# Kernel tuning notes

Measured on AMD Instinct MI355X. Metric: run time of the kernel, lower is better.

## Reference

```python
import jax, jax.numpy as jnp
import numpy as np

N, E, G = 50000, 800000, 64
IN_C, HID, HEADS, OUT_C = 128, 64, 4, 10
NEG_SLOPE = 0.2
EPS = 1e-16


def gat_conv(x, src, dst, W, a_src, a_dst, bias, heads, out_ch):
    # x: [N, F_in]; W: [F_in, heads*out_ch]; a_*: [heads, out_ch]; bias: [heads*out_ch]
    n = x.shape[0]
    h = (x @ W).reshape(n, heads, out_ch)                     # [N, H, C]
    alpha_src = jnp.einsum('nhc,hc->nh', h, a_src)            # [N, H]
    alpha_dst = jnp.einsum('nhc,hc->nh', h, a_dst)            # [N, H]
    e = jax.nn.leaky_relu(alpha_src[src] + alpha_dst[dst], NEG_SLOPE)  # [E, H]
    # segment softmax over incoming edges of each destination node
    m = jax.ops.segment_max(e, dst, num_segments=n)
    ex = jnp.exp(e - m[dst])
    denom = jax.ops.segment_sum(ex, dst, num_segments=n)
    alpha = ex / (denom[dst] + EPS)                           # [E, H]
    msg = h[src] * alpha[:, :, None]                          # [E, H, C]
    out = jax.ops.segment_sum(msg, dst, num_segments=n)       # [N, H, C]
    return out.reshape(n, heads * out_ch) + bias


def setup_inputs() -> dict:
    key = jax.random.key(0)
    ks = jax.random.split(key, 16)
    s = 0.1
    inp = {
        'x': jax.random.normal(ks[0], (N, IN_C), dtype=jnp.float32),
        'edge_index': jax.random.randint(ks[1], (2, E), 0, N, dtype=jnp.int64)
            if jax.config.jax_enable_x64 else jax.random.randint(ks[1], (2, E), 0, N).astype(jnp.int32),
        'batch': jnp.sort(jax.random.randint(ks[2], (N,), 0, G).astype(jnp.int32)),
        'W1': s * jax.random.normal(ks[3], (IN_C, HEADS * HID), dtype=jnp.float32),
        'as1': s * jax.random.normal(ks[4], (HEADS, HID), dtype=jnp.float32),
        'ad1': s * jax.random.normal(ks[5], (HEADS, HID), dtype=jnp.float32),
        'b1': jnp.zeros((HEADS * HID,), jnp.float32),
        'W2': s * jax.random.normal(ks[6], (HEADS * HID, HEADS * HID), dtype=jnp.float32),
        'as2': s * jax.random.normal(ks[7], (HEADS, HID), dtype=jnp.float32),
        'ad2': s * jax.random.normal(ks[8], (HEADS, HID), dtype=jnp.float32),
        'b2': jnp.zeros((HEADS * HID,), jnp.float32),
        'W3': s * jax.random.normal(ks[9], (HEADS * HID, HID), dtype=jnp.float32),
        'as3': s * jax.random.normal(ks[10], (1, HID), dtype=jnp.float32),
        'ad3': s * jax.random.normal(ks[11], (1, HID), dtype=jnp.float32),
        'b3': jnp.zeros((HID,), jnp.float32),
        'Wc': s * jax.random.normal(ks[12], (HID, OUT_C), dtype=jnp.float32),
        'bc': jnp.zeros((OUT_C,), jnp.float32),
    }
    return inp


def reference(x, edge_index, batch, W1, as1, ad1, b1, W2, as2, ad2, b2,
              W3, as3, ad3, b3, Wc, bc):
    n = x.shape[0]
    loop = jnp.arange(n, dtype=edge_index.dtype)
    src = jnp.concatenate([edge_index[0], loop])  # add self-loops (PyG default)
    dst = jnp.concatenate([edge_index[1], loop])

    h = gat_conv(x, src, dst, W1, as1, ad1, b1, HEADS, HID)
    h = jax.nn.elu(h)
    h = gat_conv(h, src, dst, W2, as2, ad2, b2, HEADS, HID)
    h = jax.nn.elu(h)
    h = gat_conv(h, src, dst, W3, as3, ad3, b3, 1, HID)

    # global mean pool over graphs
    sums = jax.ops.segment_sum(h, batch, num_segments=G)            # [G, HID]
    counts = jax.ops.segment_sum(jnp.ones((n,), h.dtype), batch, num_segments=G)
    pooled = sums / jnp.maximum(counts, 1.0)[:, None]

    logits = pooled @ Wc + bc                                       # [G, OUT_C]
    return logits
```

## Files before the change

kernel.cpp:

```cpp
#include <hip/hip_runtime.h>

#define NEG_SLOPE 0.2f
#define EPSV 1e-16f
#define BCAP 6144

typedef unsigned short ushort_t;
typedef unsigned char uchar_t;
typedef __attribute__((ext_vector_type(8))) short bf16x8;
typedef __attribute__((ext_vector_type(4))) float f32x4;
typedef __attribute__((ext_vector_type(2))) float f32x2;

__device__ __forceinline__ ushort_t f2bf(float f) {
    union { float f; unsigned u; } v; v.f = f;
    unsigned r = v.u + 0x7FFFu + ((v.u >> 16) & 1u);
    return (ushort_t)(r >> 16);
}
__device__ __forceinline__ float bf2f(ushort_t u) {
    union { unsigned u; float f; } v; v.u = ((unsigned)u) << 16;
    return v.f;
}
__device__ __forceinline__ uchar_t f2fp8(float f) {
    int p = __builtin_amdgcn_cvt_pk_fp8_f32(f, 0.f, 0, false);
    return (uchar_t)(p & 0xff);
}

__global__ __launch_bounds__(256)
void bucketA_kernel(const int* __restrict__ ei, int* __restrict__ gcursor,
                    unsigned* __restrict__ bbuf, int E, int n, int nbuk) {
    __shared__ int hist[256];
    __shared__ int base[256];
    const int t = threadIdx.x;
    const long cb = (long)blockIdx.x * 4096;
    const int M = E + n;
    hist[t] = 0;
    __syncthreads();
    unsigned entry[16];
    int bk[16], lr[16];
    #pragma unroll
    for (int j = 0; j < 16; ++j) {
        long i = cb + j * 256 + t;
        bk[j] = -1;
        if (i < M) {
            int s, d;
            if (i < E) { s = ei[i]; d = ei[E + i]; }
            else       { s = (int)(i - E); d = s; }
            int b = d >> 8;
            bk[j] = b;
            entry[j] = (unsigned)s | ((unsigned)(d & 255) << 16);
            lr[j] = atomicAdd(&hist[b], 1);
        }
    }
    __syncthreads();
    if (t < nbuk && hist[t] > 0) base[t] = atomicAdd(&gcursor[t], hist[t]);
    __syncthreads();
    #pragma unroll
    for (int j = 0; j < 16; ++j)
        if (bk[j] >= 0)
            bbuf[(long)bk[j] * BCAP + base[bk[j]] + lr[j]] = entry[j];
}

__global__ __launch_bounds__(256)
void bucketB1_kernel(const unsigned* __restrict__ bbuf, const int* __restrict__ gcursor,
                     int* __restrict__ deg, int n) {
    __shared__ int cnt[256];
    const int t = threadIdx.x;
    const int b = blockIdx.x;
    cnt[t] = 0;
    __syncthreads();
    const int nb = gcursor[b];
    const unsigned* bp = bbuf + (long)b * BCAP;
    for (int e = t; e < nb; e += 256)
        atomicAdd(&cnt[(bp[e] >> 16) & 255], 1);
    __syncthreads();
    int d = (b << 8) + t;
    if (d < n) deg[d] = cnt[t];
}

__global__ __launch_bounds__(1024)
void scan1_kernel(const int* __restrict__ deg, int* __restrict__ indptr,
                  int* __restrict__ bsum, int n) {
    __shared__ int wsum[16];
    const int t = threadIdx.x;
    const int lane = t & 63;
    const int w = t >> 6;
    const int i = blockIdx.x * 1024 + t;
    int v = (i < n) ? deg[i] : 0;
    int s = v;
    #pragma unroll
    for (int off = 1; off < 64; off <<= 1) {
        int u = __shfl_up(s, off);
        if (lane >= off) s += u;
    }
    if (lane == 63) wsum[w] = s;
    __syncthreads();
    if (t < 16) {
        int ws_ = wsum[t];
        #pragma unroll
        for (int off = 1; off < 16; off <<= 1) {
            int u = __shfl_up(ws_, off);
            if (t >= off) ws_ += u;
        }
        wsum[t] = ws_;
    }
    __syncthreads();
    int woff = (w > 0) ? wsum[w - 1] : 0;
    if (i < n) indptr[i + 1] = woff + s;
    if (t == 0) bsum[blockIdx.x] = wsum[15];
}

__global__ __launch_bounds__(1024)
void scan3_kernel(int* __restrict__ indptr, const int* __restrict__ bsum,
                  int nb, int n) {
    __shared__ int boff_s;
    const int t = threadIdx.x;
    if (t < 64) {
        int v = (t < nb) ? bsum[t] : 0;
        int s = v;
        #pragma unroll
        for (int off = 1; off < 64; off <<= 1) {
            int u = __shfl_up(s, off);
            if (t >= off) s += u;
        }
        if (t == (int)blockIdx.x) boff_s = s - v;
    }
    __syncthreads();
    const int boff = boff_s;
    int i = blockIdx.x * 1024 + t;
    if (i < n) indptr[i + 1] += boff;
    if (i == 0) indptr[0] = 0;
}

__global__ __launch_bounds__(256)
void bucketB2_kernel(const unsigned* __restrict__ bbuf, const int* __restrict__ gcursor,
                     const int* __restrict__ indptr, unsigned* __restrict__ csrp, int n) {
    __shared__ int cur[256];
    const int t = threadIdx.x;
    const int b = blockIdx.x;
    int d = (b << 8) + t;
    cur[t] = (d < n) ? indptr[d] : 0;
    __syncthreads();
    const int nb = gcursor[b];
    const unsigned* bp = bbuf + (long)b * BCAP;
    for (int e = t; e < nb; e += 256) {
        unsigned v = bp[e];
        int d8 = (v >> 16) & 255;
        int pos = atomicAdd(&cur[d8], 1);
        csrp[pos] = (v & 0xffffu) | ((unsigned)((b << 8) + d8) << 16);
    }
}

__global__ __launch_bounds__(256)
void prep_kernel(const float* __restrict__ x, ushort_t* __restrict__ xb, int nx4,
                 const float* __restrict__ W1, ushort_t* __restrict__ Wt1,
                 const float* __restrict__ W2, ushort_t* __restrict__ Wt2,
                 const float* __restrict__ W3, ushort_t* __restrict__ Wt3,
                 int K1, int* __restrict__ gcursor, int nbuk,
                 int* __restrict__ poolz, int gz) {
    long idx = (long)blockIdx.x * 256 + threadIdx.x;
    if (idx < nx4) {
        float4 v = *reinterpret_cast<const float4*>(&x[idx * 4]);
        ushort4 o;
        o.x = f2bf(v.x); o.y = f2bf(v.y); o.z = f2bf(v.z); o.w = f2bf(v.w);
        *reinterpret_cast<ushort4*>(&xb[idx * 4]) = o;
        return;
    }
    idx -= nx4;
    if (idx < (long)K1 * 256) {
        int c = (int)(idx % 256), k = (int)(idx / 256);
        Wt1[(long)c * K1 + k] = f2bf(W1[idx]);
        return;
    }
    idx -= (long)K1 * 256;
    if (idx < 256 * 256) {
        int c = (int)(idx % 256), k = (int)(idx / 256);
        Wt2[(long)c * 256 + k] = f2bf(W2[idx]);
        return;
    }
    idx -= 256 * 256;
    if (idx < 256 * 64) {
        int c = (int)(idx % 64), k = (int)(idx / 64);
        Wt3[(long)c * 256 + k] = f2bf(W3[idx]);
        return;
    }
    idx -= 256 * 64;
    if (idx < nbuk) { gcursor[idx] = 0; return; }
    idx -= nbuk;
    if (idx < gz) poolz[idx] = 0;
}

template<int NC>
__global__ __launch_bounds__(256)
void mfma_gemm_alpha_kernel(const ushort_t* __restrict__ A, const ushort_t* __restrict__ Wt,
                            uchar_t* __restrict__ C,
                            const float* __restrict__ a_src, const float* __restrict__ a_dst,
                            float* __restrict__ asrc, float* __restrict__ adst,
                            int M, int K, int N, int H) {
    constexpr int TBN = NC * 64;
    constexpr int MI  = (NC == 2) ? 4 : 2;
    __shared__ ushort_t As[128][40];
    __shared__ ushort_t Ws[TBN][40];
    const int tid  = threadIdx.x;
    const int w    = tid >> 6;
    const int lane = tid & 63;
    const int l15  = lane & 15;
    const int l4   = lane >> 4;
    const int row0 = blockIdx.x * 128;
    const int col0 = blockIdx.y * TBN;
    const int rbase = (NC == 2) ? (w & 1) * 64 : w * 32;
    const int cbase = (NC == 2) ? (w >> 1) * 64 : 0;

    f32x4 acc[MI][4];
    #pragma unroll
    for (int mi = 0; mi < MI; ++mi)
        #pragma unroll
        for (int ni = 0; ni < 4; ++ni)
            acc[mi][ni] = (f32x4){0.f, 0.f, 0.f, 0.f};

    for (int k0 = 0; k0 < K; k0 += 32) {
        #pragma unroll
        for (int it = 0; it < 2; ++it) {
            int idx = tid + it * 256;
            int r = idx >> 2, seg = idx & 3;
            int gr = row0 + r;
            uint4 v = make_uint4(0u, 0u, 0u, 0u);
            if (gr < M)
                v = *reinterpret_cast<const uint4*>(&A[(long)gr * K + k0 + seg * 8]);
            *reinterpret_cast<uint4*>(&As[r][seg * 8]) = v;
        }
        #pragma unroll
        for (int it = 0; it < NC; ++it) {
            int idx = tid + it * 256;
            int r = idx >> 2, seg = idx & 3;
            uint4 v = *reinterpret_cast<const uint4*>(&Wt[(long)(col0 + r) * K + k0 + seg * 8]);
            *reinterpret_cast<uint4*>(&Ws[r][seg * 8]) = v;
        }
        __syncthreads();
        bf16x8 af[MI], bfv[4];
        #pragma unroll
        for (int mi = 0; mi < MI; ++mi)
            af[mi] = *reinterpret_cast<const bf16x8*>(&As[rbase + mi * 16 + l15][8 * l4]);
        #pragma unroll
        for (int ni = 0; ni < 4; ++ni)
            bfv[ni] = *reinterpret_cast<const bf16x8*>(&Ws[cbase + ni * 16 + l15][8 * l4]);
        #pragma unroll
        for (int mi = 0; mi < MI; ++mi)
            #pragma unroll
            for (int ni = 0; ni < 4; ++ni)
                acc[mi][ni] = __builtin_amdgcn_mfma_f32_16x16x32_bf16(
                    af[mi], bfv[ni], acc[mi][ni], 0, 0, 0);
        __syncthreads();
    }

    #pragma unroll
    for (int mi = 0; mi < MI; ++mi)
        #pragma unroll
        for (int reg = 0; reg < 4; ++reg) {
            int gr = row0 + rbase + mi * 16 + l4 * 4 + reg;
            if (gr < M) {
                #pragma unroll
                for (int ni = 0; ni < 4; ++ni)
                    C[(long)gr * N + col0 + cbase + ni * 16 + l15] = f2fp8(acc[mi][ni][reg]);
            }
        }

    const int hd = (col0 + cbase) >> 6;
    float aS[4], aD[4];
    #pragma unroll
    for (int ni = 0; ni < 4; ++ni) {
        aS[ni] = a_src[hd * 64 + ni * 16 + l15];
        aD[ni] = a_dst[hd * 64 + ni * 16 + l15];
    }
    #pragma unroll
    for (int mi = 0; mi < MI; ++mi)
        #pragma unroll
        for (int reg = 0; reg < 4; ++reg) {
            float s = 0.f, d = 0.f;
            #pragma unroll
            for (int ni = 0; ni < 4; ++ni) {
                s += acc[mi][ni][reg] * aS[ni];
                d += acc[mi][ni][reg] * aD[ni];
            }
            #pragma unroll
            for (int off = 1; off < 16; off <<= 1) {
                s += __shfl_xor(s, off);
                d += __shfl_xor(d, off);
            }
            int gr = row0 + rbase + mi * 16 + l4 * 4 + reg;
            if (l15 == 0 && gr < M) {
                asrc[gr * H + hd] = s;
                adst[gr * H + hd] = d;
            }
        }
}

__global__ __launch_bounds__(256)
void edgeexp4_kernel(const unsigned* __restrict__ csrp,
                     const float4* __restrict__ asrc4, const float4* __restrict__ adst4,
                     float4* __restrict__ ex4, int M) {
    int i = blockIdx.x * blockDim.x + threadIdx.x;
    if (i >= M) return;
    unsigned v = csrp[i];
    int s = (int)(v & 0xffffu), d = (int)(v >> 16);
    float4 a = asrc4[s];
    float4 b = adst4[d];
    float e, ex_, ey_, ez_, ew_;
    e = a.x + b.x; e = e > 0.f ? e : NEG_SLOPE * e; ex_ = __expf(e);
    e = a.y + b.y; e = e > 0.f ? e : NEG_SLOPE * e; ey_ = __expf(e);
    e = a.z + b.z; e = e > 0.f ? e : NEG_SLOPE * e; ez_ = __expf(e);
    e = a.w + b.w; e = e > 0.f ? e : NEG_SLOPE * e; ew_ = __expf(e);
    ex4[i] = make_float4(ex_, ey_, ez_, ew_);
}

__global__ __launch_bounds__(256)
void edgeexp1_kernel(const unsigned* __restrict__ csrp,
                     const float* __restrict__ asrc, const float* __restrict__ adst,
                     float* __restrict__ ex1, int M) {
    int i = blockIdx.x * blockDim.x + threadIdx.x;
    if (i >= M) return;
    unsigned v = csrp[i];
    float e = asrc[v & 0xffffu] + adst[v >> 16];
    e = e > 0.f ? e : NEG_SLOPE * e;
    ex1[i] = __expf(e);
}

__global__ __launch_bounds__(256)
void aggregate4_kernel(const uchar_t* __restrict__ h, const float* __restrict__ ex4,
                       const int* __restrict__ indptr, const unsigned* __restrict__ csrp,
                       const float* __restrict__ bias, ushort_t* __restrict__ out,
                       int n, int apply_elu) {
    const int node = (blockIdx.x * blockDim.x + threadIdx.x) >> 6;
    const int lane = threadIdx.x & 63;
    if (node >= n) return;
    const int hd  = lane >> 4;
    const int beg = indptr[node], end = indptr[node + 1];
    const int cnt = end - beg;
    const uchar_t* __restrict__ hrow = h + 4 * lane;
    const float* __restrict__ exh = ex4 + 4 * (long)beg + hd;

    float sum_ex = 0.f;
    float ax = 0.f, ay = 0.f, az = 0.f, aw = 0.f;
    int i = 0;
    for (; i + 8 <= cnt; i += 8) {
        long s[8];
        float ee[8];
        unsigned v[8];
        #pragma unroll
        for (int u = 0; u < 8; ++u) s[u] = (long)(csrp[beg + i + u] & 0xffffu);
        #pragma unroll
        for (int u = 0; u < 8; ++u) ee[u] = exh[(long)(i + u) * 4];
        #pragma unroll
        for (int u = 0; u < 8; ++u)
            v[u] = *reinterpret_cast<const unsigned*>(hrow + (s[u] << 8));
        #pragma unroll
        for (int u = 0; u < 8; ++u) {
            f32x2 lo = __builtin_amdgcn_cvt_pk_f32_fp8((int)v[u], false);
            f32x2 hi = __builtin_amdgcn_cvt_pk_f32_fp8((int)v[u], true);
            sum_ex += ee[u];
            ax += ee[u] * lo[0];
            ay += ee[u] * lo[1];
            az += ee[u] * hi[0];
            aw += ee[u] * hi[1];
        }
    }
    for (; i < cnt; ++i) {
        long s = (long)(csrp[beg + i] & 0xffffu);
        float ee = exh[(long)i * 4];
        unsigned v = *reinterpret_cast<const unsigned*>(hrow + (s << 8));
        f32x2 lo = __builtin_amdgcn_cvt_pk_f32_fp8((int)v, false);
        f32x2 hi = __builtin_amdgcn_cvt_pk_f32_fp8((int)v, true);
        sum_ex += ee;
        ax += ee * lo[0]; ay += ee * lo[1];
        az += ee * hi[0]; aw += ee * hi[1];
    }
    const float inv = 1.f / (sum_ex + EPSV);
    float4 b4 = *reinterpret_cast<const float4*>(bias + 4 * lane);
    float ox = ax * inv + b4.x;
    float oy = ay * inv + b4.y;
    float oz = az * inv + b4.z;
    float ow = aw * inv + b4.w;
    if (apply_elu) {
        ox = ox > 0.f ? ox : expm1f(ox);
        oy = oy > 0.f ? oy : expm1f(oy);
        oz = oz > 0.f ? oz : expm1f(oz);
        ow = ow > 0.f ? ow : expm1f(ow);
    }
    ushort4 o4;
    o4.x = f2bf(ox); o4.y = f2bf(oy); o4.z = f2bf(oz); o4.w = f2bf(ow);
    *reinterpret_cast<ushort4*>(out + (long)node * 256 + 4 * lane) = o4;
}

__global__ __launch_bounds__(256)
void aggregate_kernel(const uchar_t* __restrict__ h, const float* __restrict__ ex1,
                      const int* __restrict__ indptr, const unsigned* __restrict__ csrp,
                      const float* __restrict__ bias, ushort_t* __restrict__ out,
                      int n, int apply_elu) {
    const int node = (blockIdx.x * blockDim.x + threadIdx.x) >> 6;
    const int lane = threadIdx.x & 63;
    if (node >= n) return;
    const int beg = indptr[node], end = indptr[node + 1];
    const int cnt = end - beg;
    const uchar_t* __restrict__ hh = h + lane;

    float sum_ex = 0.f, acc = 0.f;
    int i = 0;
    for (; i + 8 <= cnt; i += 8) {
        long s[8];
        float ee[8];
        uchar_t b[8];
        #pragma unroll
        for (int u = 0; u < 8; ++u) s[u] = (long)(csrp[beg + i + u] & 0xffffu);
        #pragma unroll
        for (int u = 0; u < 8; ++u) ee[u] = ex1[beg + i + u];
        #pragma unroll
        for (int u = 0; u < 8; ++u) b[u] = hh[s[u] << 6];
        #pragma unroll
        for (int u = 0; u < 8; ++u) {
            f32x2 r = __builtin_amdgcn_cvt_pk_f32_fp8((int)b[u], false);
            sum_ex += ee[u];
            acc += ee[u] * r[0];
        }
    }
    for (; i < cnt; ++i) {
        long s = (long)(csrp[beg + i] & 0xffffu);
        float ee = ex1[beg + i];
        f32x2 r = __builtin_amdgcn_cvt_pk_f32_fp8((int)hh[s << 6], false);
        sum_ex += ee;
        acc += ee * r[0];
    }
    float o = acc / (sum_ex + EPSV) + bias[lane];
    if (apply_elu) o = o > 0.f ? o : expm1f(o);
    out[(long)node * 64 + lane] = f2bf(o);
}

constexpr int POOL_CHUNK = 128;

__global__ __launch_bounds__(64)
void pool_kernel(const ushort_t* __restrict__ h, const int* __restrict__ batch,
                 float* __restrict__ sums, int* __restrict__ counts, int n) {
    int lane = threadIdx.x;
    int start = blockIdx.x * POOL_CHUNK;
    if (start >= n) return;
    int end = min(start + POOL_CHUNK, n);
    int gcur = batch[start];
    float acc = 0.f;
    int run = 0;
    for (int i = start; i < end; ++i) {
        int g = batch[i];
        if (g != gcur) {
            atomicAdd(&sums[gcur * 64 + lane], acc);
            if (lane == 0) atomicAdd(&counts[gcur], run);
            acc = 0.f; run = 0; gcur = g;
        }
        acc += bf2f(h[(long)i * 64 + lane]);
        ++run;
    }
    atomicAdd(&sums[gcur * 64 + lane], acc);
    if (lane == 0) atomicAdd(&counts[gcur], run);
}

__global__ void classify_kernel(const float* __restrict__ sums, const int* __restrict__ counts,
                                const float* __restrict__ Wc, const float* __restrict__ bc,
                                float* __restrict__ out, int G) {
    int t = threadIdx.x;
    if (t >= G * 10) return;
    int g = t / 10, o = t - g * 10;
    int c_ = counts[g];
    float inv = 1.f / (float)(c_ > 1 ? c_ : 1);
    float acc = bc[o];
    for (int c = 0; c < 64; ++c)
        acc += sums[g * 64 + c] * inv * Wc[c * 10 + o];
    out[t] = acc;
}

extern "C" void kernel_launch(void* const* d_in, const int* in_sizes, int n_in,
                              void* d_out, int out_size, void* d_ws, size_t ws_size,
                              hipStream_t stream) {
    const float* x   = (const float*)d_in[0];
    const int*   ei  = (const int*)d_in[1];
    const int*   bat = (const int*)d_in[2];
    const float* W1  = (const float*)d_in[3];
    const float* as1 = (const float*)d_in[4];
    const float* ad1 = (const float*)d_in[5];
    const float* b1  = (const float*)d_in[6];
    const float* W2  = (const float*)d_in[7];
    const float* as2 = (const float*)d_in[8];
    const float* ad2 = (const float*)d_in[9];
    const float* b2  = (const float*)d_in[10];
    const float* W3  = (const float*)d_in[11];
    const float* as3 = (const float*)d_in[12];
    const float* ad3 = (const float*)d_in[13];
    const float* b3  = (const float*)d_in[14];
    const float* Wc  = (const float*)d_in[15];
    const float* bc  = (const float*)d_in[16];
    float* out = (float*)d_out;

    const int N = in_sizes[2];
    const int E = in_sizes[1] / 2;
    const int M = E + N;
    const int IN_C = in_sizes[0] / N;
    const int G = out_size / 10;
    const int NBUK = (N + 255) >> 8;

    char* p = (char*)d_ws;
    auto carve = [&](size_t bytes) -> void* {
        void* r = (void*)p;
        p += (bytes + 255) & ~(size_t)255;
        return r;
    };
    uchar_t*  hA  = (uchar_t*)carve((size_t)N * 256);
    ushort_t* hB  = (ushort_t*)carve((size_t)N * 256 * 2);
    size_t xb_ex_bytes = (size_t)M * 16;
    size_t xb_need = (size_t)N * IN_C * 2;
    if (xb_need > xb_ex_bytes) xb_ex_bytes = xb_need;
    ushort_t* xb  = (ushort_t*)carve(xb_ex_bytes);
    float*    ex  = (float*)xb;
    ushort_t* Wt1 = (ushort_t*)carve((size_t)256 * IN_C * 2);
    ushort_t* Wt2 = (ushort_t*)carve((size_t)256 * 256 * 2);
    ushort_t* Wt3 = (ushort_t*)carve((size_t)64 * 256 * 2);
    float* asrc = (float*)carve((size_t)N * 4 * 4);
    float* adst = (float*)carve((size_t)N * 4 * 4);
    float* sums = (float*)carve((size_t)G * 64 * 4 + (size_t)G * 4);
    int*   cnts = (int*)(sums + (size_t)G * 64);
    unsigned* bbuf = (unsigned*)carve((size_t)NBUK * BCAP * 4);
    int*   gcursor = (int*)carve((size_t)NBUK * 4);
    int*   deg  = (int*)carve((size_t)N * 4);
    int*   iptr = (int*)carve((size_t)(N + 1) * 4);
    unsigned* csrp = (unsigned*)carve((size_t)M * 4);
    int*   bsum = (int*)carve(256 * 4);
    (void)ws_size; (void)n_in;

    const int NB = (N + 1023) / 1024;
    const int MB = (M + 255) / 256;
    const int AGB = (N + 3) / 4;

    {
        long nx4 = (long)N * IN_C / 4;
        int gz = G * 65;
        long total = nx4 + (long)IN_C * 256 + 256 * 256 + 256 * 64 + NBUK + gz;
        prep_kernel<<<(int)((total + 255) / 256), 256, 0, stream>>>(
            x, xb, (int)nx4, W1, Wt1, W2, Wt2, W3, Wt3, IN_C, gcursor, NBUK, (int*)sums, gz);
    }

    bucketA_kernel<<<(M + 4095) / 4096, 256, 0, stream>>>(ei, gcursor, bbuf, E, N, NBUK);
    bucketB1_kernel<<<NBUK, 256, 0, stream>>>(bbuf, gcursor, deg, N);
    scan1_kernel<<<NB, 1024, 0, stream>>>(deg, iptr, bsum, N);
    scan3_kernel<<<NB, 1024, 0, stream>>>(iptr, bsum, NB, N);
    bucketB2_kernel<<<NBUK, 256, 0, stream>>>(bbuf, gcursor, iptr, csrp, N);

    {
        dim3 grid((N + 127) / 128, 2);
        mfma_gemm_alpha_kernel<2><<<grid, 256, 0, stream>>>(xb, Wt1, hA, as1, ad1,
                                                            asrc, adst, N, IN_C, 256, 4);
    }
    edgeexp4_kernel<<<MB, 256, 0, stream>>>(csrp, (const float4*)asrc,
                                            (const float4*)adst, (float4*)ex, M);
    aggregate4_kernel<<<AGB, 256, 0, stream>>>(hA, ex, iptr, csrp, b1, hB, N, 1);

    {
        dim3 grid((N + 127) / 128, 2);
        mfma_gemm_alpha_kernel<2><<<grid, 256, 0, stream>>>(hB, Wt2, hA, as2, ad2,
                                                            asrc, adst, N, 256, 256, 4);
    }
    edgeexp4_kernel<<<MB, 256, 0, stream>>>(csrp, (const float4*)asrc,
                                            (const float4*)adst, (float4*)ex, M);
    aggregate4_kernel<<<AGB, 256, 0, stream>>>(hA, ex, iptr, csrp, b2, hB, N, 1);

    {
        dim3 grid((N + 127) / 128, 1);
        mfma_gemm_alpha_kernel<1><<<grid, 256, 0, stream>>>(hB, Wt3, hA, as3, ad3,
                                                            asrc, adst, N, 256, 64, 1);
    }
    edgeexp1_kernel<<<MB, 256, 0, stream>>>(csrp, asrc, adst, ex, M);
    aggregate_kernel<<<AGB, 256, 0, stream>>>(hA, ex, iptr, csrp, b3, hB, N, 0);

    pool_kernel<<<(N + POOL_CHUNK - 1) / POOL_CHUNK, 64, 0, stream>>>(hB, bat, sums, cnts, N);
    classify_kernel<<<1, 640, 0, stream>>>(sums, cnts, Wc, bc, out, G);
}
```

Measured before the change: 393.4 us.

## Fuse CSR degree count and scan into bucket pass; use buffer loads in aggregate

Measured after the change: 392.5 us. No clear change (-0.2%).

```diff
diff --git a/kernel.cpp b/kernel.cpp
--- a/kernel.cpp
+++ b/kernel.cpp
@@ -3,6 +3,12 @@
 #define NEG_SLOPE 0.2f
 #define EPSV 1e-16f
 #define BCAP 6144
+
+#if defined(__has_builtin)
+#if __has_builtin(__builtin_amdgcn_make_buffer_rsrc) && __has_builtin(__builtin_amdgcn_raw_buffer_load_b32)
+#define USE_BUFLOAD 1
+#endif
+#endif
 
 typedef unsigned short ushort_t;
 typedef unsigned char uchar_t;
@@ -60,10 +66,39 @@
 }
 
 __global__ __launch_bounds__(256)
-void bucketB1_kernel(const unsigned* __restrict__ bbuf, const int* __restrict__ gcursor,
-                     int* __restrict__ deg, int n) {
+void scanb_kernel(const int* __restrict__ gcursor, int* __restrict__ bbase, int nbuk) {
+    __shared__ int wsum[4];
+    const int t = threadIdx.x;
+    const int lane = t & 63;
+    const int w = t >> 6;
+    int v = (t < nbuk) ? gcursor[t] : 0;
+    int s = v;
+    #pragma unroll
+    for (int off = 1; off < 64; off <<= 1) {
+        int u = __shfl_up(s, off);
+        if (lane >= off) s += u;
+    }
+    if (lane == 63) wsum[w] = s;
+    __syncthreads();
+    if (t == 0) {
+        int r = 0;
+        #pragma unroll
+        for (int j = 0; j < 4; ++j) { int c = wsum[j]; wsum[j] = r; r += c; }
+    }
+    __syncthreads();
+    if (t < nbuk) bbase[t] = s - v + wsum[w];
+}
+
+__global__ __launch_bounds__(256)
+void bucketB2_kernel(const unsigned* __restrict__ bbuf, const int* __restrict__ gcursor,
+                     const int* __restrict__ bbase, int* __restrict__ iptr,
+                     unsigned* __restrict__ csrp, int n) {
     __shared__ int cnt[256];
+    __shared__ int wsum[4];
+    __shared__ int cur[256];
     const int t = threadIdx.x;
+    const int lane = t & 63;
+    const int w = t >> 6;
     const int b = blockIdx.x;
     cnt[t] = 0;
     __syncthreads();
@@ -72,19 +107,7 @@
     for (int e = t; e < nb; e += 256)
         atomicAdd(&cnt[(bp[e] >> 16) & 255], 1);
     __syncthreads();
-    int d = (b << 8) + t;
-    if (d < n) deg[d] = cnt[t];
-}
-
-__global__ __launch_bounds__(1024)
-void scan1_kernel(const int* __restrict__ deg, int* __restrict__ indptr,
-                  int* __restrict__ bsum, int n) {
-    __shared__ int wsum[16];
-    const int t = threadIdx.x;
-    const int lane = t & 63;
-    const int w = t >> 6;
-    const int i = blockIdx.x * 1024 + t;
-    int v = (i < n) ? deg[i] : 0;
+    int v = cnt[t];
     int s = v;
     #pragma unroll
     for (int off = 1; off < 64; off <<= 1) {
@@ -93,59 +116,23 @@
     }
     if (lane == 63) wsum[w] = s;
     __syncthreads();
-    if (t < 16) {
-        int ws_ = wsum[t];
-        #pragma unroll
-        for (int off = 1; off < 16; off <<= 1) {
-            int u = __shfl_up(ws_, off);
-            if (t >= off) ws_ += u;
-        }
-        wsum[t] = ws_;
-    }
-    __syncthreads();
-    int woff = (w > 0) ? wsum[w - 1] : 0;
-    if (i < n) indptr[i + 1] = woff + s;
-    if (t == 0) bsum[blockIdx.x] = wsum[15];
-}
-
-__global__ __launch_bounds__(1024)
-void scan3_kernel(int* __restrict__ indptr, const int* __restrict__ bsum,
-                  int nb, int n) {
-    __shared__ int boff_s;
-    const int t = threadIdx.x;
-    if (t < 64) {
-        int v = (t < nb) ? bsum[t] : 0;
-        int s = v;
-        #pragma unroll
-        for (int off = 1; off < 64; off <<= 1) {
-            int u = __shfl_up(s, off);
-            if (t >= off) s += u;
-        }
-        if (t == (int)blockIdx.x) boff_s = s - v;
-    }
-    __syncthreads();
-    const int boff = boff_s;
-    int i = blockIdx.x * 1024 + t;
-    if (i < n) indptr[i + 1] += boff;
-    if (i == 0) indptr[0] = 0;
-}
-
-__global__ __launch_bounds__(256)
-void bucketB2_kernel(const unsigned* __restrict__ bbuf, const int* __restrict__ gcursor,
-                     const int* __restrict__ indptr, unsigned* __restrict__ csrp, int n) {
-    __shared__ int cur[256];
-    const int t = threadIdx.x;
-    const int b = blockIdx.x;
-    int d = (b << 8) + t;
-    cur[t] = (d < n) ? indptr[d] : 0;
-    __syncthreads();
-    const int nb = gcursor[b];
-    const unsigned* bp = bbuf + (long)b * BCAP;
+    if (t == 0) {
+        int r = 0;
+        #pragma unroll
+        for (int j = 0; j < 4; ++j) { int c = wsum[j]; wsum[j] = r; r += c; }
+    }
+    __syncthreads();
+    const int start = bbase[b] + s - v + wsum[w];
+    const int d = (b << 8) + t;
+    if (d < n) iptr[d] = start;
+    if (d == n - 1) iptr[n] = start + v;
+    cur[t] = start;
+    __syncthreads();
     for (int e = t; e < nb; e += 256) {
-        unsigned v = bp[e];
-        int d8 = (v >> 16) & 255;
+        unsigned vv = bp[e];
+        int d8 = (vv >> 16) & 255;
         int pos = atomicAdd(&cur[d8], 1);
-        csrp[pos] = (v & 0xffffu) | ((unsigned)((b << 8) + d8) << 16);
+        csrp[pos] = (vv & 0xffffu) | ((unsigned)((b << 8) + d8) << 16);
     }
 }
 
@@ -334,23 +321,33 @@
     const int hd  = lane >> 4;
     const int beg = indptr[node], end = indptr[node + 1];
     const int cnt = end - beg;
+#ifdef USE_BUFLOAD
+    __amdgpu_buffer_rsrc_t hrs = __builtin_amdgcn_make_buffer_rsrc(
+        const_cast<uchar_t*>(h), (short)0, n * 256, 0x00020000);
+    const int vbase = 4 * lane;
+#else
     const uchar_t* __restrict__ hrow = h + 4 * lane;
+#endif
     const float* __restrict__ exh = ex4 + 4 * (long)beg + hd;
 
     float sum_ex = 0.f;
     float ax = 0.f, ay = 0.f, az = 0.f, aw = 0.f;
     int i = 0;
     for (; i + 8 <= cnt; i += 8) {
-        long s[8];
+        int s[8];
         float ee[8];
         unsigned v[8];
         #pragma unroll
-        for (int u = 0; u < 8; ++u) s[u] = (long)(csrp[beg + i + u] & 0xffffu);
-        #pragma unroll
-        for (int u = 0; u < 8; ++u) ee[u] = exh[(long)(i + u) * 4];
+        for (int u = 0; u < 8; ++u) s[u] = (int)(csrp[beg + i + u] & 0xffffu);
+        #pragma unroll
+        for (int u = 0; u < 8; ++u) ee[u] = exh[4 * (i + u)];
         #pragma unroll
         for (int u = 0; u < 8; ++u)
-            v[u] = *reinterpret_cast<const unsigned*>(hrow + (s[u] << 8));
+#ifdef USE_BUFLOAD
+            v[u] = (unsigned)__builtin_amdgcn_raw_buffer_load_b32(hrs, (s[u] << 8) + vbase, 0, 0);
+#else
+            v[u] = *reinterpret_cast<const unsigned*>(hrow + ((long)s[u] << 8));
+#endif
         #pragma unroll
         for (int u = 0; u < 8; ++u) {
             f32x2 lo = __builtin_amdgcn_cvt_pk_f32_fp8((int)v[u], false);
@@ -363,9 +360,14 @@
         }
     }
     for (; i < cnt; ++i) {
-        long s = (long)(csrp[beg + i] & 0xffffu);
-        float ee = exh[(long)i * 4];
-        unsigned v = *reinterpret_cast<const unsigned*>(hrow + (s << 8));
+        int s = (int)(csrp[beg + i] & 0xffffu);
+        float ee = exh[4 * i];
+        unsigned v;
+#ifdef USE_BUFLOAD
+        v = (unsigned)__builtin_amdgcn_raw_buffer_load_b32(hrs, (s << 8) + vbase, 0, 0);
+#else
+        v = *reinterpret_cast<const unsigned*>(hrow + ((long)s << 8));
+#endif
         f32x2 lo = __builtin_amdgcn_cvt_pk_f32_fp8((int)v, false);
         f32x2 hi = __builtin_amdgcn_cvt_pk_f32_fp8((int)v, true);
         sum_ex += ee;
@@ -404,11 +406,11 @@
     float sum_ex = 0.f, acc = 0.f;
     int i = 0;
     for (; i + 8 <= cnt; i += 8) {
-        long s[8];
+        int s[8];
         float ee[8];
         uchar_t b[8];
         #pragma unroll
-        for (int u = 0; u < 8; ++u) s[u] = (long)(csrp[beg + i + u] & 0xffffu);
+        for (int u = 0; u < 8; ++u) s[u] = (int)(csrp[beg + i + u] & 0xffffu);
         #pragma unroll
         for (int u = 0; u < 8; ++u) ee[u] = ex1[beg + i + u];
         #pragma unroll
@@ -421,7 +423,7 @@
         }
     }
     for (; i < cnt; ++i) {
-        long s = (long)(csrp[beg + i] & 0xffffu);
+        int s = (int)(csrp[beg + i] & 0xffffu);
         float ee = ex1[beg + i];
         f32x2 r = __builtin_amdgcn_cvt_pk_f32_fp8((int)hh[s << 6], false);
         sum_ex += ee;
@@ -523,13 +525,11 @@
     int*   cnts = (int*)(sums + (size_t)G * 64);
     unsigned* bbuf = (unsigned*)carve((size_t)NBUK * BCAP * 4);
     int*   gcursor = (int*)carve((size_t)NBUK * 4);
-    int*   deg  = (int*)carve((size_t)N * 4);
+    int*   bbase   = (int*)carve((size_t)NBUK * 4);
     int*   iptr = (int*)carve((size_t)(N + 1) * 4);
     unsigned* csrp = (unsigned*)carve((size_t)M * 4);
-    int*   bsum = (int*)carve(256 * 4);
     (void)ws_size; (void)n_in;
 
-    const int NB = (N + 1023) / 1024;
     const int MB = (M + 255) / 256;
     const int AGB = (N + 3) / 4;
 
@@ -542,10 +542,8 @@
     }
 
     bucketA_kernel<<<(M + 4095) / 4096, 256, 0, stream>>>(ei, gcursor, bbuf, E, N, NBUK);
-    bucketB1_kernel<<<NBUK, 256, 0, stream>>>(bbuf, gcursor, deg, N);
-    scan1_kernel<<<NB, 1024, 0, stream>>>(deg, iptr, bsum, N);
-    scan3_kernel<<<NB, 1024, 0, stream>>>(iptr, bsum, NB, N);
-    bucketB2_kernel<<<NBUK, 256, 0, stream>>>(bbuf, gcursor, iptr, csrp, N);
+    scanb_kernel<<<1, 256, 0, stream>>>(gcursor, bbase, NBUK);
+    bucketB2_kernel<<<NBUK, 256, 0, stream>>>(bbuf, gcursor, bbase, iptr, csrp, N);
 
     {
         dim3 grid((N + 127) / 128, 2);
```
